# Performance work log

Measured on AMD Instinct MI355X. Metric: run time of the kernel, lower is better.

## Reference

```python
import jax, jax.numpy as jnp
import numpy as np

N = 50000      # nodes
E = 800000     # edges
NUM_STATIC = 8
T = 24         # dynamic seq len (in_features - num_static)
LH = 64        # lstm_hidden
C = 32         # n_hidden (per-head out channels)
H = 4          # heads
NC = 4         # num_classes
IN_GAT = LH + NUM_STATIC  # 72


def _uniform(key, shape, scale):
    return jax.random.uniform(key, shape, jnp.float32, -scale, scale)


def setup_inputs() -> dict:
    key = jax.random.key(0)
    ks = jax.random.split(key, 32)
    s1 = 1.0 / np.sqrt(LH)
    inp = {
        'x': jax.random.normal(ks[0], (N, NUM_STATIC + T), jnp.float32),
        'edge_index': jax.random.randint(ks[1], (2, E), 0, N, jnp.int64),
        'edge_attr': jax.random.uniform(ks[2], (E, 1), jnp.float32),
        # LSTM layer 0 (input_size=1), layer 1 (input_size=LH); gate order i,f,g,o
        'w_ih0': _uniform(ks[3], (4 * LH, 1), s1),
        'w_hh0': _uniform(ks[4], (4 * LH, LH), s1),
        'b_ih0': _uniform(ks[5], (4 * LH,), s1),
        'b_hh0': _uniform(ks[6], (4 * LH,), s1),
        'w_ih1': _uniform(ks[7], (4 * LH, LH), s1),
        'w_hh1': _uniform(ks[8], (4 * LH, LH), s1),
        'b_ih1': _uniform(ks[9], (4 * LH,), s1),
        'b_hh1': _uniform(ks[10], (4 * LH,), s1),
        # GATConv params (PyG: glorot lin, att vectors; bias zeros-init but randomize)
        'lin_w': _uniform(ks[11], (H * C, IN_GAT), np.sqrt(6.0 / (IN_GAT + H * C))),
        'lin_edge_w': _uniform(ks[12], (H * C, 1), np.sqrt(6.0 / (1 + H * C))),
        'att_src': _uniform(ks[13], (H, C), np.sqrt(6.0 / (C + 1))),
        'att_dst': _uniform(ks[14], (H, C), np.sqrt(6.0 / (C + 1))),
        'att_edge': _uniform(ks[15], (H, C), np.sqrt(6.0 / (C + 1))),
        'gat_bias': _uniform(ks[16], (H * C,), 0.1),
        # final Linear
        'fc_w': _uniform(ks[17], (NC, H * C), 1.0 / np.sqrt(H * C)),
        'fc_b': _uniform(ks[18], (NC,), 1.0 / np.sqrt(H * C)),
    }
    return inp


def _lstm_layer(x_seq, w_ih, w_hh, b_ih, b_hh):
    # x_seq: [N, T, D] -> hs: [N, T, LH]
    xw = jnp.einsum('ntd,gd->ntg', x_seq, w_ih) + b_ih + b_hh  # [N,T,4LH]
    n = x_seq.shape[0]
    h0 = jnp.zeros((n, w_hh.shape[1]), x_seq.dtype)

    def step(carry, xt):
        h, c = carry
        g = xt + h @ w_hh.T
        i, f, gg, o = jnp.split(g, 4, axis=-1)
        c = jax.nn.sigmoid(f) * c + jax.nn.sigmoid(i) * jnp.tanh(gg)
        h = jax.nn.sigmoid(o) * jnp.tanh(c)
        return (h, c), h

    _, hs = jax.lax.scan(step, (h0, h0), jnp.swapaxes(xw, 0, 1))
    return jnp.swapaxes(hs, 0, 1)


def reference(x, edge_index, edge_attr,
              w_ih0, w_hh0, b_ih0, b_hh0, w_ih1, w_hh1, b_ih1, b_hh1,
              lin_w, lin_edge_w, att_src, att_dst, att_edge, gat_bias,
              fc_w, fc_b):
    static = x[:, :NUM_STATIC]
    dyn = x[:, NUM_STATIC:, None]                      # [N,T,1]
    h1 = _lstm_layer(dyn, w_ih0, w_hh0, b_ih0, b_hh0)  # [N,T,LH] (eval: no dropout)
    h2 = _lstm_layer(h1, w_ih1, w_hh1, b_ih1, b_hh1)
    combined = jnp.concatenate([h2[:, -1, :], static], axis=1)  # [N, LH+NUM_STATIC]

    # --- GATConv (PyG defaults: add_self_loops=True, fill_value='mean') ---
    n = combined.shape[0]
    loop = jnp.arange(n, dtype=edge_index.dtype)
    src = jnp.concatenate([edge_index[0], loop])
    dst = jnp.concatenate([edge_index[1], loop])
    ea_mean = jnp.mean(edge_attr, axis=0, keepdims=True)        # [1,1]
    ea = jnp.concatenate([edge_attr, jnp.broadcast_to(ea_mean, (n, 1))], axis=0)

    xl = (combined @ lin_w.T).reshape(n, H, C)                  # [N,H,C]
    a_src = jnp.einsum('nhc,hc->nh', xl, att_src)               # [N,H]
    a_dst = jnp.einsum('nhc,hc->nh', xl, att_dst)
    e_emb = (ea @ lin_edge_w.T).reshape(-1, H, C)               # [Et,H,C]
    a_edge = jnp.einsum('ehc,hc->eh', e_emb, att_edge)          # [Et,H]

    logits = jax.nn.leaky_relu(a_src[src] + a_dst[dst] + a_edge, 0.2)  # [Et,H]
    m = jax.ops.segment_max(logits, dst, num_segments=n)
    ex = jnp.exp(logits - m[dst])
    denom = jax.ops.segment_sum(ex, dst, num_segments=n)
    alpha = ex / (denom[dst] + 1e-16)                           # [Et,H] (eval: no dropout)

    msg = xl[src] * alpha[:, :, None]                           # [Et,H,C]
    out = jax.ops.segment_sum(msg, dst, num_segments=n)         # [N,H,C]
    out = out.reshape(n, H * C) + gat_bias

    out = jax.nn.elu(out)
    return jax.nn.relu(out @ fc_w.T + fc_b)                     # [N,NC]
```

## Files before the change

### kernel.cpp

```cpp
#include <hip/hip_runtime.h>
#include <cstdint>

#define TT 24

typedef _Float16 half8 __attribute__((ext_vector_type(8)));
typedef float f32x4 __attribute__((ext_vector_type(4)));

static __device__ __forceinline__ float fsig(float x){
  float e = __builtin_amdgcn_exp2f(-1.44269504f*x);
  return __builtin_amdgcn_rcpf(1.0f + e);
}
static __device__ __forceinline__ float ftanh(float x){
  float e = __builtin_amdgcn_exp2f(-2.88539008f*x);
  return fmaf(2.0f, __builtin_amdgcn_rcpf(1.0f + e), -1.0f);
}
static __device__ __forceinline__ float lrelu(float x){ return x > 0.f ? x : 0.2f*x; }

static __device__ __forceinline__ int swzh(int b){ return b ^ (((b>>7)&7)<<4); }
static __device__ __forceinline__ float h2f_lo(unsigned u){
  union { unsigned short s; _Float16 f; } c; c.s = (unsigned short)(u & 0xFFFF); return (float)c.f;
}
static __device__ __forceinline__ float h2f_hi(unsigned u){
  union { unsigned short s; _Float16 f; } c; c.s = (unsigned short)(u >> 16); return (float)c.f;
}

__global__ void kPrep(const float* __restrict__ w_hh0, const float* __restrict__ w_ih1,
                      const float* __restrict__ w_hh1, const float* __restrict__ lin_w,
                      const float* __restrict__ lin_edge_w, const float* __restrict__ att_edge,
                      unsigned short* __restrict__ Bf,
                      float* __restrict__ linwT, float* __restrict__ cE)
{
  int gid = blockIdx.x*256 + threadIdx.x;
  if (gid < 49152){
    int mat = gid / 16384;
    int r = gid - mat*16384;
    int c = r>>13, nt = (r>>9)&15, l = (r>>3)&63, j = r&7;
    int k = c*32 + (l>>4)*8 + j;
    int col = nt*16 + (l&15);
    const float* wsrc = (mat==0) ? w_hh0 : (mat==1 ? w_ih1 : w_hh1);
    float v = wsrc[col*64 + k];
    union { _Float16 f; unsigned short u; } cv;
    cv.f = (_Float16)v;
    Bf[gid] = cv.u;
  }
  int g2 = gid - 49152;
  if (g2 >= 0 && g2 < 72*128){
    int k = g2 >> 7, ch = g2 & 127;
    linwT[g2] = lin_w[ch*72 + k];
  }
  if (gid >= 58368 && gid < 58372){
    int h = gid - 58368;
    float s = 0.f;
    for (int c=0;c<32;c++) s += lin_edge_w[h*32+c]*att_edge[h*32+c];
    cE[h] = s;
  }
}

__global__ __launch_bounds__(256) void kAB(const float* __restrict__ x,
    const unsigned short* __restrict__ Bf,
    const float* __restrict__ w_ih0, const float* __restrict__ b_ih0, const float* __restrict__ b_hh0,
    const float* __restrict__ b_ih1, const float* __restrict__ b_hh1,
    float* __restrict__ h2last, int N)
{
  __shared__ __align__(16) unsigned short sH1[2048];
  __shared__ __align__(16) unsigned short sH2[2048];
  __shared__ float sX[32*25];
  const int tid = threadIdx.x;
  const int wq = tid>>6, l = tid&63;
  const int lr = l&15, lg = l>>4;
  const int nb = blockIdx.x*32;

  for (int i=tid;i<768;i+=256){
    int m = i/24, tt = i - m*24;
    int n = nb + m;
    sX[m*25+tt] = (n<N) ? x[(size_t)n*32 + 8 + tt] : 0.f;
  }
  for (int i=tid;i<2048;i+=256){ sH1[i]=0; sH2[i]=0; }

  half8 w0[2][4], w1i[2][4], w1h[2][4];
  #pragma unroll
  for (int c=0;c<2;c++){
    #pragma unroll
    for (int nt=0;nt<4;nt++){
      w0 [c][nt] = *(const half8*)&Bf[(( 0 + c*16 + nt*4 + wq)<<9) + l*8];
      w1i[c][nt] = *(const half8*)&Bf[((32 + c*16 + nt*4 + wq)<<9) + l*8];
      w1h[c][nt] = *(const half8*)&Bf[((64 + c*16 + nt*4 + wq)<<9) + l*8];
    }
  }

  float wih[4], bb0[4], bb1[4];
  #pragma unroll
  for (int nt=0;nt<4;nt++){
    int col = nt*64 + wq*16 + lr;
    wih[nt] = w_ih0[col];
    bb0[nt] = b_ih0[col] + b_hh0[col];
    bb1[nt] = b_ih1[col] + b_hh1[col];
  }
  float cc0[8], cc1[8];
  #pragma unroll
  for (int i=0;i<8;i++){ cc0[i]=0.f; cc1[i]=0.f; }
  __syncthreads();

  const char* h1B = (const char*)sH1;
  const char* h2B = (const char*)sH2;

  for (int t=0;t<TT;t++){
    f32x4 acc[2][4];
    #pragma unroll
    for (int mt=0;mt<2;mt++){
      #pragma unroll
      for (int r=0;r<4;r++){
        float xv = sX[(mt*16 + lg*4 + r)*25 + t];
        #pragma unroll
        for (int nt=0;nt<4;nt++) acc[mt][nt][r] = fmaf(xv, wih[nt], bb0[nt]);
      }
    }
    #pragma unroll
    for (int c=0;c<2;c++){
      half8 a[2];
      #pragma unroll
      for (int mt=0;mt<2;mt++)
        a[mt] = *(const half8*)(h1B + swzh((mt*16+lr)*128 + c*64 + lg*16));
      #pragma unroll
      for (int nt=0;nt<4;nt++){
        #pragma unroll
        for (int mt=0;mt<2;mt++)
          acc[mt][nt] = __builtin_amdgcn_mfma_f32_16x16x32_f16(a[mt], w0[c][nt], acc[mt][nt], 0,0,0);
      }
    }
    __syncthreads();
    #pragma unroll
    for (int mt=0;mt<2;mt++){
      #pragma unroll
      for (int r=0;r<4;r++){
        int idx = mt*4+r, nd = mt*16 + lg*4 + r;
        float ig = fsig(acc[mt][0][r]), fg = fsig(acc[mt][1][r]);
        float gg = ftanh(acc[mt][2][r]), og = fsig(acc[mt][3][r]);
        cc0[idx] = fg*cc0[idx] + ig*gg;
        float h = og*ftanh(cc0[idx]);
        union { _Float16 f; unsigned short u; } cv; cv.f = (_Float16)h;
        *(unsigned short*)((char*)sH1 + swzh(nd*128 + (wq*16+lr)*2)) = cv.u;
      }
    }
    __syncthreads();
    #pragma unroll
    for (int mt=0;mt<2;mt++)
      #pragma unroll
      for (int nt=0;nt<4;nt++)
        #pragma unroll
        for (int r=0;r<4;r++) acc[mt][nt][r] = bb1[nt];
    #pragma unroll
    for (int c4=0;c4<4;c4++){
      const char* srcA = (c4<2) ? h1B : h2B;
      const int cc = c4&1;
      half8 a[2];
      #pragma unroll
      for (int mt=0;mt<2;mt++)
        a[mt] = *(const half8*)(srcA + swzh((mt*16+lr)*128 + cc*64 + lg*16));
      #pragma unroll
      for (int nt=0;nt<4;nt++){
        half8 b = (c4<2) ? w1i[cc][nt] : w1h[cc][nt];
        #pragma unroll
        for (int mt=0;mt<2;mt++)
          acc[mt][nt] = __builtin_amdgcn_mfma_f32_16x16x32_f16(a[mt], b, acc[mt][nt], 0,0,0);
      }
    }
    __syncthreads();
    #pragma unroll
    for (int mt=0;mt<2;mt++){
      #pragma unroll
      for (int r=0;r<4;r++){
        int idx = mt*4+r, nd = mt*16 + lg*4 + r;
        float ig = fsig(acc[mt][0][r]), fg = fsig(acc[mt][1][r]);
        float gg = ftanh(acc[mt][2][r]), og = fsig(acc[mt][3][r]);
        cc1[idx] = fg*cc1[idx] + ig*gg;
        float h = og*ftanh(cc1[idx]);
        union { _Float16 f; unsigned short u; } cv; cv.f = (_Float16)h;
        *(unsigned short*)((char*)sH2 + swzh(nd*128 + (wq*16+lr)*2)) = cv.u;
        if (t == TT-1){
          int n = nb + nd;
          if (n < N) h2last[(size_t)n*64 + wq*16 + lr] = h;
        }
      }
    }
  }
}

__global__ __launch_bounds__(256) void kXL(const float* __restrict__ h2last, const float* __restrict__ x,
    const float* __restrict__ linwT, const float* __restrict__ att_src, const float* __restrict__ att_dst,
    unsigned short* __restrict__ xlh, float* __restrict__ a_src, float* __restrict__ a_dst, int N)
{
  __shared__ float sLW[72*128];
  __shared__ float sC[16*72];
  const int tid = threadIdx.x;
  const int nb0 = blockIdx.x * 16;
  for (int i = tid*4; i < 9216; i += 1024)
    *(float4*)&sLW[i] = *(const float4*)&linwT[i];
  for (int i = tid; i < 16*64; i += 256){
    int m = i >> 6, k = i & 63; int n = nb0 + m;
    sC[m*72 + k] = (n < N) ? h2last[(size_t)n*64 + k] : 0.f;
  }
  if (tid < 128){
    int m = tid >> 3, j = tid & 7; int n = nb0 + m;
    sC[m*72 + 64 + j] = (n < N) ? x[(size_t)n*32 + j] : 0.f;
  }
  __syncthreads();
  const int ch = tid & 127, half = tid >> 7;
  float acc[8];
  #pragma unroll
  for (int m=0;m<8;m++) acc[m]=0.f;
  for (int k=0;k<72;k++){
    float w = sLW[k*128 + ch];
    #pragma unroll
    for (int m=0;m<8;m++) acc[m] += w * sC[(half*8+m)*72 + k];
  }
  float aS = att_src[ch], aD = att_dst[ch];
  int h = ch >> 5;
  #pragma unroll
  for (int m=0;m<8;m++){
    int n = nb0 + half*8 + m;
    float v = acc[m];
    float ps = v*aS, pd = v*aD;
    #pragma unroll
    for (int d=1; d<32; d<<=1){ ps += __shfl_xor(ps, d); pd += __shfl_xor(pd, d); }
    if (n < N){
      union { _Float16 f; unsigned short u; } cv; cv.f = (_Float16)v;
      xlh[(size_t)n*128 + (ch&63)*2 + (ch>>6)] = cv.u;
      if ((ch & 31) == 0){ a_src[n*4 + h] = ps; a_dst[n*4 + h] = pd; }
    }
  }
}

__global__ void kEa(const float* __restrict__ ea, float* __restrict__ acc, int E){
  int gid = blockIdx.x*blockDim.x + threadIdx.x;
  float s = 0.f;
  for (int i = gid; i < E; i += gridDim.x*blockDim.x) s += ea[i];
  #pragma unroll
  for (int d=1; d<64; d<<=1) s += __shfl_xor(s, d);
  if ((threadIdx.x & 63) == 0) atomicAdd(acc, s);
}

__global__ void kDeg(const int* __restrict__ dst, int* __restrict__ deg, int E, int N){
  int e = blockIdx.x*256 + threadIdx.x;
  if (e < E){
    unsigned d = (unsigned)dst[e];
    if (d < (unsigned)N) atomicAdd(&deg[d], 1);
  }
}

__global__ __launch_bounds__(1024) void kScan(const int* __restrict__ deg, int* __restrict__ ptrA,
                                              int* __restrict__ cursor, int N){
  __shared__ int sWS[16];
  __shared__ int sWO[16];
  const int tid = threadIdx.x;
  const int C = (N + 1 + 1023) / 1024;
  const int i0 = tid * C;
  int local = 0;
  for (int i = i0; i < i0 + C && i < N; i++) local += deg[i];
  int lane = tid & 63, wv = tid >> 6;
  int v = local;
  #pragma unroll
  for (int d=1; d<64; d<<=1){ int u = __shfl_up(v, d); if (lane >= d) v += u; }
  if (lane == 63) sWS[wv] = v;
  __syncthreads();
  if (tid < 16){
    int s = sWS[tid];
    int vv = s;
    #pragma unroll
    for (int d=1; d<16; d<<=1){ int u = __shfl_up(vv, d); if (tid >= d) vv += u; }
    sWO[tid] = vv - s;
  }
  __syncthreads();
  int run = sWO[wv] + (v - local);
  for (int i = i0; i < i0 + C; i++){
    if (i <= N){
      ptrA[i] = run;
      if (i < N){ cursor[i] = run; run += deg[i]; }
    }
  }
}

__global__ void kFill(const int* __restrict__ dst, int* __restrict__ cursor,
                      int* __restrict__ csr, int E, int N){
  int e = blockIdx.x*256 + threadIdx.x;
  if (e < E){
    unsigned d = (unsigned)dst[e];
    if (d < (unsigned)N){ int p = atomicAdd(&cursor[d], 1); csr[p] = e; }
  }
}

__global__ __launch_bounds__(256) void kAgg(const unsigned short* __restrict__ xlh,
    const float* __restrict__ a_src,
    const float* __restrict__ a_dst, const int* __restrict__ esrc, const float* __restrict__ eattr,
    const int* __restrict__ ptrA, const int* __restrict__ csr, const float* __restrict__ cE,
    const float* __restrict__ eacc, const float* __restrict__ gat_bias, const float* __restrict__ fc_w,
    const float* __restrict__ fc_b, float* __restrict__ out, int N, int E)
{
  const int n = blockIdx.x*4 + (threadIdx.x >> 6);
  const int lane = threadIdx.x & 63;
  if (n >= N) return;
  const unsigned* xlp = (const unsigned*)xlh;
  float4 cEv = *(const float4*)cE;
  float eam = eacc[0] / (float)E;
  float4 ad  = *(const float4*)&a_dst[n*4];
  float4 asn = *(const float4*)&a_src[n*4];
  float sl0 = lrelu(asn.x + ad.x + eam*cEv.x);
  float sl1 = lrelu(asn.y + ad.y + eam*cEv.y);
  float sl2 = lrelu(asn.z + ad.z + eam*cEv.z);
  float sl3 = lrelu(asn.w + ad.w + eam*cEv.w);
  float mx0=sl0, mx1=sl1, mx2=sl2, mx3=sl3;
  const int p0 = ptrA[n], p1 = ptrA[n+1];
  for (int i = p0 + lane; i < p1; i += 64){
    int e = csr[i];
    int s = esrc[e];
    float ev = eattr[e];
    float4 av = *(const float4*)&a_src[s*4];
    mx0 = fmaxf(mx0, lrelu(av.x + ad.x + ev*cEv.x));
    mx1 = fmaxf(mx1, lrelu(av.y + ad.y + ev*cEv.y));
    mx2 = fmaxf(mx2, lrelu(av.z + ad.z + ev*cEv.z));
    mx3 = fmaxf(mx3, lrelu(av.w + ad.w + ev*cEv.w));
  }
  #pragma unroll
  for (int d=1; d<64; d<<=1){
    mx0 = fmaxf(mx0, __shfl_xor(mx0,d));
    mx1 = fmaxf(mx1, __shfl_xor(mx1,d));
    mx2 = fmaxf(mx2, __shfl_xor(mx2,d));
    mx3 = fmaxf(mx3, __shfl_xor(mx3,d));
  }
  const int ch0 = lane, ch1 = lane + 64;
  const int h0 = lane >> 5;
  float adh0 = h0 ? ad.y : ad.x,  adh1 = h0 ? ad.w : ad.z;
  float ceh0 = h0 ? cEv.y : cEv.x, ceh1 = h0 ? cEv.w : cEv.z;
  float mxh0 = h0 ? mx1 : mx0,    mxh1 = h0 ? mx3 : mx2;
  float slh0 = h0 ? sl1 : sl0,    slh1 = h0 ? sl3 : sl2;
  float pse0 = __expf(slh0 - mxh0), pse1 = __expf(slh1 - mxh1);
  float den0 = pse0, den1 = pse1;
  unsigned un = xlp[(size_t)n*64 + lane];
  float acc0 = pse0 * h2f_lo(un);
  float acc1 = pse1 * h2f_hi(un);
  for (int i = p0; i < p1; i++){
    int e = csr[i];
    int s = esrc[e];
    float ev = eattr[e];
    float4 av = *(const float4*)&a_src[s*4];
    float avh0 = h0 ? av.y : av.x;
    float avh1 = h0 ? av.w : av.z;
    float pp0 = __expf(lrelu(avh0 + adh0 + ev*ceh0) - mxh0);
    float pp1 = __expf(lrelu(avh1 + adh1 + ev*ceh1) - mxh1);
    den0 += pp0; den1 += pp1;
    unsigned u = xlp[(size_t)s*64 + lane];
    acc0 += pp0 * h2f_lo(u);
    acc1 += pp1 * h2f_hi(u);
  }
  float v0 = acc0/(den0 + 1e-16f) + gat_bias[ch0];
  float v1 = acc1/(den1 + 1e-16f) + gat_bias[ch1];
  v0 = v0 > 0.f ? v0 : __expf(v0) - 1.f;
  v1 = v1 > 0.f ? v1 : __expf(v1) - 1.f;
  #pragma unroll
  for (int o=0;o<4;o++){
    float p = fc_w[o*128 + ch0]*v0 + fc_w[o*128 + ch1]*v1;
    #pragma unroll
    for (int d=1; d<64; d<<=1) p += __shfl_xor(p, d);
    if (lane == 0) out[(size_t)n*4 + o] = fmaxf(p + fc_b[o], 0.f);
  }
}

extern "C" void kernel_launch(void* const* d_in, const int* in_sizes, int n_in,
                              void* d_out, int out_size, void* d_ws, size_t ws_size,
                              hipStream_t stream)
{
  (void)n_in; (void)out_size; (void)ws_size;
  const float* x          = (const float*)d_in[0];
  const int*   eidx       = (const int*)d_in[1];
  const float* eattr      = (const float*)d_in[2];
  const float* w_ih0      = (const float*)d_in[3];
  const float* w_hh0      = (const float*)d_in[4];
  const float* b_ih0      = (const float*)d_in[5];
  const float* b_hh0      = (const float*)d_in[6];
  const float* w_ih1      = (const float*)d_in[7];
  const float* w_hh1      = (const float*)d_in[8];
  const float* b_ih1      = (const float*)d_in[9];
  const float* b_hh1      = (const float*)d_in[10];
  const float* lin_w      = (const float*)d_in[11];
  const float* lin_edge_w = (const float*)d_in[12];
  const float* att_src    = (const float*)d_in[13];
  const float* att_dst    = (const float*)d_in[14];
  const float* att_edge   = (const float*)d_in[15];
  const float* gat_bias   = (const float*)d_in[16];
  const float* fc_w       = (const float*)d_in[17];
  const float* fc_b       = (const float*)d_in[18];
  float* out = (float*)d_out;

  const int N = in_sizes[0] / 32;
  const int E = in_sizes[1] / 2;
  const int* esrc = eidx;
  const int* edst = eidx + E;

  float* ws = (float*)d_ws;
  size_t o = 0;
  unsigned short* Bfrag = (unsigned short*)(ws + o); o += 24576;
  float* linwT  = ws + o; o += 72*128;
  float* cE     = ws + o; o += 4;
  float* eacc   = ws + o; o += 4;
  float* h2last = ws + o; o += (size_t)N*64;
  unsigned short* xlh = (unsigned short*)(ws + o); o += (size_t)N*64;
  float* a_src  = ws + o; o += (size_t)N*4;
  float* a_dst  = ws + o; o += (size_t)N*4;
  int* deg      = (int*)(ws + o); o += (size_t)N;
  int* ptrA     = (int*)(ws + o); o += (size_t)N + 1;
  int* cursor   = (int*)(ws + o); o += (size_t)N;
  int* csr      = (int*)(ws + o); o += (size_t)E;

  hipMemsetAsync(deg, 0, (size_t)N*4, stream);
  hipMemsetAsync(eacc, 0, 4, stream);
  kPrep<<<229, 256, 0, stream>>>(w_hh0, w_ih1, w_hh1, lin_w, lin_edge_w, att_edge,
                                 Bfrag, linwT, cE);
  kEa<<<512, 256, 0, stream>>>(eattr, eacc, E);
  kDeg<<<(E+255)/256, 256, 0, stream>>>(edst, deg, E, N);
  kScan<<<1, 1024, 0, stream>>>(deg, ptrA, cursor, N);
  kFill<<<(E+255)/256, 256, 0, stream>>>(edst, cursor, csr, E, N);

  kAB<<<(N+31)/32, 256, 0, stream>>>(x, Bfrag, w_ih0, b_ih0, b_hh0,
                                     b_ih1, b_hh1, h2last, N);

  kXL<<<(N+15)/16, 256, 0, stream>>>(h2last, x, linwT, att_src, att_dst, xlh, a_src, a_dst, N);
  kAgg<<<(N+3)/4, 256, 0, stream>>>(xlh, a_src, a_dst, esrc, eattr, ptrA, csr, cE, eacc,
                                    gat_bias, fc_w, fc_b, out, N, E);
}
```

Baseline: 865.8 us.

## Double-buffer LSTM hidden states and pack two node tiles per block

The fused two-layer LSTM kernel now double-buffers the layer-1 and layer-2 hidden-state tiles in shared memory. This cuts the barriers per timestep from four to two, since reads come from the current buffer and writes go to the next. Each block now runs two independent 32-node tiles with 512 threads, which halves the grid size and doubles shared memory use per block. The aim is less barrier stall in the serial recurrence, at the cost of more LDS and fewer, larger blocks, which could hurt occupancy or load balance.

```diff
diff --git a/kernel.cpp b/kernel.cpp
--- a/kernel.cpp
+++ b/kernel.cpp
@@ -56,26 +56,34 @@
   }
 }
 
-__global__ __launch_bounds__(256) void kAB(const float* __restrict__ x,
+__global__ __launch_bounds__(512) void kAB(const float* __restrict__ x,
     const unsigned short* __restrict__ Bf,
     const float* __restrict__ w_ih0, const float* __restrict__ b_ih0, const float* __restrict__ b_hh0,
     const float* __restrict__ b_ih1, const float* __restrict__ b_hh1,
     float* __restrict__ h2last, int N)
 {
-  __shared__ __align__(16) unsigned short sH1[2048];
-  __shared__ __align__(16) unsigned short sH2[2048];
-  __shared__ float sX[32*25];
+  __shared__ __align__(16) unsigned short sH1[2][2][2048];
+  __shared__ __align__(16) unsigned short sH2[2][2][2048];
+  __shared__ float sX[2][800];
   const int tid = threadIdx.x;
-  const int wq = tid>>6, l = tid&63;
+  const int wid = tid>>6, l = tid&63;
+  const int tile = wid>>2, wq = wid&3;
   const int lr = l&15, lg = l>>4;
-  const int nb = blockIdx.x*32;
-
-  for (int i=tid;i<768;i+=256){
-    int m = i/24, tt = i - m*24;
-    int n = nb + m;
-    sX[m*25+tt] = (n<N) ? x[(size_t)n*32 + 8 + tt] : 0.f;
-  }
-  for (int i=tid;i<2048;i+=256){ sH1[i]=0; sH2[i]=0; }
+  const int nb = blockIdx.x*64 + tile*32;
+
+  for (int i=tid;i<1600;i+=512){
+    int tl = i/800, r = i - tl*800;
+    int m = r/25, tt = r - m*25;
+    if (tt < 24){
+      int n = blockIdx.x*64 + tl*32 + m;
+      sX[tl][m*25+tt] = (n<N) ? x[(size_t)n*32 + 8 + tt] : 0.f;
+    }
+  }
+  {
+    unsigned short* f1 = &sH1[0][0][0];
+    unsigned short* f2 = &sH2[0][0][0];
+    for (int i=tid;i<8192;i+=512){ f1[i]=0; f2[i]=0; }
+  }
 
   half8 w0[2][4], w1i[2][4], w1h[2][4];
   #pragma unroll
@@ -101,16 +109,19 @@
   for (int i=0;i<8;i++){ cc0[i]=0.f; cc1[i]=0.f; }
   __syncthreads();
 
-  const char* h1B = (const char*)sH1;
-  const char* h2B = (const char*)sH2;
-
   for (int t=0;t<TT;t++){
+    const int cur = t&1, nxt = cur^1;
+    const char* h1c = (const char*)sH1[tile][cur];
+    const char* h2c = (const char*)sH2[tile][cur];
+    char* h1n = (char*)sH1[tile][nxt];
+    char* h2n = (char*)sH2[tile][nxt];
+
     f32x4 acc[2][4];
     #pragma unroll
     for (int mt=0;mt<2;mt++){
       #pragma unroll
       for (int r=0;r<4;r++){
-        float xv = sX[(mt*16 + lg*4 + r)*25 + t];
+        float xv = sX[tile][(mt*16 + lg*4 + r)*25 + t];
         #pragma unroll
         for (int nt=0;nt<4;nt++) acc[mt][nt][r] = fmaf(xv, wih[nt], bb0[nt]);
       }
@@ -120,7 +131,7 @@
       half8 a[2];
       #pragma unroll
       for (int mt=0;mt<2;mt++)
-        a[mt] = *(const half8*)(h1B + swzh((mt*16+lr)*128 + c*64 + lg*16));
+        a[mt] = *(const half8*)(h1c + swzh((mt*16+lr)*128 + c*64 + lg*16));
       #pragma unroll
       for (int nt=0;nt<4;nt++){
         #pragma unroll
@@ -128,7 +139,6 @@
           acc[mt][nt] = __builtin_amdgcn_mfma_f32_16x16x32_f16(a[mt], w0[c][nt], acc[mt][nt], 0,0,0);
       }
     }
-    __syncthreads();
     #pragma unroll
     for (int mt=0;mt<2;mt++){
       #pragma unroll
@@ -139,7 +149,7 @@
         cc0[idx] = fg*cc0[idx] + ig*gg;
         float h = og*ftanh(cc0[idx]);
         union { _Float16 f; unsigned short u; } cv; cv.f = (_Float16)h;
-        *(unsigned short*)((char*)sH1 + swzh(nd*128 + (wq*16+lr)*2)) = cv.u;
+        *(unsigned short*)(h1n + swzh(nd*128 + (wq*16+lr)*2)) = cv.u;
       }
     }
     __syncthreads();
@@ -151,7 +161,7 @@
         for (int r=0;r<4;r++) acc[mt][nt][r] = bb1[nt];
     #pragma unroll
     for (int c4=0;c4<4;c4++){
-      const char* srcA = (c4<2) ? h1B : h2B;
+      const char* srcA = (c4<2) ? (const char*)h1n : h2c;
       const int cc = c4&1;
       half8 a[2];
       #pragma unroll
@@ -165,7 +175,6 @@
           acc[mt][nt] = __builtin_amdgcn_mfma_f32_16x16x32_f16(a[mt], b, acc[mt][nt], 0,0,0);
       }
     }
-    __syncthreads();
     #pragma unroll
     for (int mt=0;mt<2;mt++){
       #pragma unroll
@@ -176,13 +185,14 @@
         cc1[idx] = fg*cc1[idx] + ig*gg;
         float h = og*ftanh(cc1[idx]);
         union { _Float16 f; unsigned short u; } cv; cv.f = (_Float16)h;
-        *(unsigned short*)((char*)sH2 + swzh(nd*128 + (wq*16+lr)*2)) = cv.u;
+        *(unsigned short*)(h2n + swzh(nd*128 + (wq*16+lr)*2)) = cv.u;
         if (t == TT-1){
           int n = nb + nd;
           if (n < N) h2last[(size_t)n*64 + wq*16 + lr] = h;
         }
       }
     }
+    __syncthreads();
   }
 }
 
@@ -420,7 +430,7 @@
   kScan<<<1, 1024, 0, stream>>>(deg, ptrA, cursor, N);
   kFill<<<(E+255)/256, 256, 0, stream>>>(edst, cursor, csr, E, N);
 
-  kAB<<<(N+31)/32, 256, 0, stream>>>(x, Bfrag, w_ih0, b_ih0, b_hh0,
+  kAB<<<(N+63)/64, 512, 0, stream>>>(x, Bfrag, w_ih0, b_ih0, b_hh0,
                                      b_ih1, b_hh1, h2last, N);
 
   kXL<<<(N+15)/16, 256, 0, stream>>>(h2last, x, linwT, att_src, att_dst, xlh, a_src, a_dst, N);
```

Result: faster. 837.1 us (-3.3%).
